# Optimization experiments

Measured on AMD Instinct MI355X. Metric: run time of the kernel, lower is better.

The kernel has to match this reference:

```python
import jax, jax.numpy as jnp
import numpy as np

B, S, D = 32, 4096, 512

def setup_inputs() -> dict:
    key = jax.random.key(0)
    ks = jax.random.split(key, 5)
    scale = 1.0 / np.sqrt(D)
    return {
        "query": jax.random.normal(ks[0], (B, D), jnp.float32),
        "values": jax.random.normal(ks[1], (B, S, D), jnp.float32),
        "W1": jax.random.normal(ks[2], (D, D), jnp.float32) * scale,
        "b1": jnp.zeros((D,), jnp.float32),
        "W2": jax.random.normal(ks[3], (D, D), jnp.float32) * scale,
        "b2": jnp.zeros((D,), jnp.float32),
        "V": jax.random.normal(ks[4], (D, 1), jnp.float32) * scale,
        "bv": jnp.zeros((1,), jnp.float32),
    }

def reference(query, values, W1, b1, W2, b2, V, bv):
    # query: [B, D], values: [B, S, D]
    q_proj = query @ W1 + b1                      # [B, D]
    v_proj = jnp.einsum('bsd,de->bse', values, W2) + b2  # [B, S, D]
    hidden = jnp.tanh(q_proj[:, None, :] + v_proj)       # [B, S, D]
    score = jnp.einsum('bsd,de->bse', hidden, V) + bv    # [B, S, 1]
    attn = jax.nn.softmax(score, axis=1)                 # softmax over seq axis
    context = jnp.sum(attn * values, axis=1)             # [B, D]
    return (context, attn)
```

## Files before the change

kernel.cpp:

```cpp
#include <hip/hip_runtime.h>
#include <hip/hip_bf16.h>
#include <stdint.h>

#define NB 32
#define NS 4096
#define ND 512

typedef __attribute__((ext_vector_type(8))) short short8;
typedef __attribute__((ext_vector_type(4))) float floatx4;

__device__ __forceinline__ short f2bf(float f) {
    unsigned int u = __builtin_bit_cast(unsigned int, f);
    return (short)((u + 0x8000u) >> 16);
}

__device__ __forceinline__ float fast_tanh(float x) {
    float e = __expf(2.0f * x);
    return 1.0f - 2.0f * __builtin_amdgcn_rcpf(e + 1.0f);
}

__device__ __forceinline__ short8 pack8(float4 a, float4 b) {
    short8 w;
    w[0] = f2bf(a.x); w[1] = f2bf(a.y); w[2] = f2bf(a.z); w[3] = f2bf(a.w);
    w[4] = f2bf(b.x); w[5] = f2bf(b.y); w[6] = f2bf(b.z); w[7] = f2bf(b.w);
    return w;
}

__global__ void __launch_bounds__(256) qproj_kernel(
    const float* __restrict__ query, const float* __restrict__ W1,
    const float* __restrict__ b1, const float* __restrict__ b2,
    float* __restrict__ qb) {
    int b = blockIdx.x;
    int t = threadIdx.x;
    __shared__ float q[ND];
    q[t] = query[b * ND + t];
    q[t + 256] = query[b * ND + t + 256];
    __syncthreads();
    float acc0 = 0.f, acc1 = 0.f;
#pragma unroll 8
    for (int k = 0; k < ND; k++) {
        float qk = q[k];
        acc0 += qk * W1[k * ND + t];
        acc1 += qk * W1[k * ND + t + 256];
    }
    qb[b * ND + t] = acc0 + b1[t] + b2[t];
    qb[b * ND + t + 256] = acc1 + b1[t + 256] + b2[t + 256];
}

__global__ void __launch_bounds__(256) w2t_kernel(
    const float* __restrict__ W2, unsigned short* __restrict__ W2Tt) {
    int g = blockIdx.x * 256 + threadIdx.x;
    int nt = g >> 14;
    int ks = (g >> 10) & 15;
    int kq = (g >> 8) & 3;
    int n  = g & 255;
    int e  = nt * 256 + n;
    int k0 = ks * 32 + kq * 8;
    short8 v;
#pragma unroll
    for (int j = 0; j < 8; j++)
        v[j] = f2bf(W2[(size_t)(k0 + j) * ND + e]);
    *(short8*)&W2Tt[(size_t)g * 8] = v;
}

__global__ void __launch_bounds__(256, 2) scores_kernel(
    const float* __restrict__ values, const unsigned short* __restrict__ W2Tt,
    const float* __restrict__ qb, const float* __restrict__ V,
    float* __restrict__ scores) {
    const int nt = blockIdx.x;
    const int st = blockIdx.y;
    const int b  = blockIdx.z;
    const int n0 = nt * 256, s0 = st * 128;

    __shared__ __align__(16) unsigned short sA[2][4096];
    __shared__ __align__(16) unsigned short sB[2][8192];
    __shared__ float sQb[256];
    __shared__ float sV[256];

    const int tid  = threadIdx.x;
    const int lane = tid & 63;
    const int wave = tid >> 6;
    const int wr = wave >> 1, wc = wave & 1;
    const int mr = lane & 15;
    const int q  = lane >> 4;

    sQb[tid] = qb[b * ND + n0 + tid];
    sV[tid]  = V[n0 + tid];

    floatx4 acc[4][8] = {};

    const int arow = tid >> 1, ah = tid & 1;
    const float* arow_ptr = values + ((size_t)b * NS + s0 + arow) * ND + ah * 16;
    const int awr0 = (2 * ah * 128 + arow) * 8;
    const int awr1 = ((2 * ah + 1) * 128 + arow) * 8;

    const unsigned short* bsrc0 = W2Tt + (size_t)(nt * 16) * 8192;

    const int aoff = (q * 128 + wr * 64 + mr) * 8;
    const int boff = (q * 256 + wc * 128 + mr) * 8;

    {
#pragma unroll
        for (int r = 0; r < 4; r++) {
            int c = tid + 256 * r;
            __builtin_amdgcn_global_load_lds(
                (const __attribute__((address_space(1))) unsigned int*)(bsrc0 + c * 8),
                (__attribute__((address_space(3))) unsigned int*)&sB[0][c * 8],
                16, 0, 0);
        }
        const float4* ap = (const float4*)arow_ptr;
        float4 x0 = ap[0], x1 = ap[1], x2 = ap[2], x3 = ap[3];
        *(short8*)&sA[0][awr0] = pack8(x0, x1);
        *(short8*)&sA[0][awr1] = pack8(x2, x3);
    }
    __syncthreads();

    for (int ks = 0; ks < 16; ks++) {
        const int cur = ks & 1, nxt = cur ^ 1;
        float4 x0, x1, x2, x3;
        if (ks < 15) {
            const unsigned short* bsrc = bsrc0 + (size_t)(ks + 1) * 8192;
#pragma unroll
            for (int r = 0; r < 4; r++) {
                int c = tid + 256 * r;
                __builtin_amdgcn_global_load_lds(
                    (const __attribute__((address_space(1))) unsigned int*)(bsrc + c * 8),
                    (__attribute__((address_space(3))) unsigned int*)&sB[nxt][c * 8],
                    16, 0, 0);
            }
            const float4* ap = (const float4*)(arow_ptr + (ks + 1) * 32);
            x0 = ap[0]; x1 = ap[1]; x2 = ap[2]; x3 = ap[3];
        }

        short8 af[4], bfr[8];
#pragma unroll
        for (int i = 0; i < 4; i++) af[i]  = *(const short8*)&sA[cur][aoff + i * 128];
#pragma unroll
        for (int j = 0; j < 8; j++) bfr[j] = *(const short8*)&sB[cur][boff + j * 128];
#pragma unroll
        for (int i = 0; i < 4; i++)
#pragma unroll
            for (int j = 0; j < 8; j++)
                acc[i][j] = __builtin_amdgcn_mfma_f32_16x16x32_bf16(af[i], bfr[j], acc[i][j], 0, 0, 0);

        if (ks < 15) {
            *(short8*)&sA[nxt][awr0] = pack8(x0, x1);
            *(short8*)&sA[nxt][awr1] = pack8(x2, x3);
        }
        __syncthreads();
    }

    float vcoef[8], qadd[8];
#pragma unroll
    for (int j = 0; j < 8; j++) {
        int col = wc * 128 + j * 16 + mr;
        vcoef[j] = sV[col];
        qadd[j]  = sQb[col];
    }

#pragma unroll
    for (int i = 0; i < 4; i++) {
#pragma unroll
        for (int r = 0; r < 4; r++) {
            float p = 0.f;
#pragma unroll
            for (int j = 0; j < 8; j++)
                p += fast_tanh(acc[i][j][r] + qadd[j]) * vcoef[j];
            p += __shfl_xor(p, 1);
            p += __shfl_xor(p, 2);
            p += __shfl_xor(p, 4);
            p += __shfl_xor(p, 8);
            if (mr == 0) {
                int row = wr * 64 + i * 16 + q * 4 + r;
                atomicAdd(&scores[(size_t)b * NS + s0 + row], p);
            }
        }
    }
}

__global__ void __launch_bounds__(256) softmax_kernel(
    const float* __restrict__ scores, float* __restrict__ attn) {
    int b = blockIdx.x;
    int t = threadIdx.x;
    __shared__ float red[4];
    __shared__ float bcast[2];
    const float* sc = scores + (size_t)b * NS;
    float v[16];
    float m = -1e30f;
#pragma unroll
    for (int i = 0; i < 16; i++) { v[i] = sc[t + i * 256]; m = fmaxf(m, v[i]); }
    for (int o = 32; o; o >>= 1) m = fmaxf(m, __shfl_xor(m, o));
    if ((t & 63) == 0) red[t >> 6] = m;
    __syncthreads();
    if (t == 0) bcast[0] = fmaxf(fmaxf(red[0], red[1]), fmaxf(red[2], red[3]));
    __syncthreads();
    m = bcast[0];
    float sum = 0.f;
#pragma unroll
    for (int i = 0; i < 16; i++) { v[i] = __expf(v[i] - m); sum += v[i]; }
    for (int o = 32; o; o >>= 1) sum += __shfl_xor(sum, o);
    if ((t & 63) == 0) red[t >> 6] = sum;
    __syncthreads();
    if (t == 0) bcast[1] = red[0] + red[1] + red[2] + red[3];
    __syncthreads();
    float inv = 1.0f / bcast[1];
    float* ao = attn + (size_t)b * NS;
#pragma unroll
    for (int i = 0; i < 16; i++) ao[t + i * 256] = v[i] * inv;
}

__global__ void __launch_bounds__(256) context_partial_kernel(
    const float* __restrict__ values, const float* __restrict__ attn,
    float* __restrict__ pctx) {
    int sc = blockIdx.x;
    int b  = blockIdx.y;
    int t  = threadIdx.x;
    __shared__ float sAttn[512];
    sAttn[t]       = attn[(size_t)b * NS + sc * 512 + t];
    sAttn[t + 256] = attn[(size_t)b * NS + sc * 512 + t + 256];
    __syncthreads();
    int d = t * 2;
    const float2* vp = (const float2*)(values + ((size_t)b * NS + sc * 512) * ND + d);
    float ax = 0.f, ay = 0.f;
#pragma unroll 8
    for (int s = 0; s < 512; s++) {
        float a = sAttn[s];
        float2 v = vp[(size_t)s * 256];
        ax += a * v.x; ay += a * v.y;
    }
    pctx[((size_t)sc * 32 + b) * ND + d]     = ax;
    pctx[((size_t)sc * 32 + b) * ND + d + 1] = ay;
}

__global__ void __launch_bounds__(256) context_reduce_kernel(
    const float* __restrict__ pctx, float* __restrict__ ctx) {
    int i = blockIdx.x * 256 + threadIdx.x;
    float s = 0.f;
#pragma unroll
    for (int p = 0; p < 8; p++) s += pctx[(size_t)p * (32 * ND) + i];
    ctx[i] = s;
}

extern "C" void kernel_launch(void* const* d_in, const int* in_sizes, int n_in,
                              void* d_out, int out_size, void* d_ws, size_t ws_size,
                              hipStream_t stream) {
    const float* query  = (const float*)d_in[0];
    const float* values = (const float*)d_in[1];
    const float* W1     = (const float*)d_in[2];
    const float* b1     = (const float*)d_in[3];
    const float* W2     = (const float*)d_in[4];
    const float* b2     = (const float*)d_in[5];
    const float* V      = (const float*)d_in[6];

    float* ctx_out  = (float*)d_out;
    float* attn_out = (float*)d_out + NB * ND;

    char* ws = (char*)d_ws;
    float*          qb     = (float*)ws;
    unsigned short* W2Tt   = (unsigned short*)(ws + (64 << 10));
    float*          scores = (float*)(ws + (64 << 10) + (512 << 10));
    float*          pctx   = (float*)(ws + (64 << 10) + (1024 << 10));

    hipMemsetAsync(scores, 0, (size_t)NB * NS * sizeof(float), stream);

    qproj_kernel<<<NB, 256, 0, stream>>>(query, W1, b1, b2, qb);
    w2t_kernel<<<128, 256, 0, stream>>>(W2, W2Tt);
    scores_kernel<<<dim3(2, 32, 32), 256, 0, stream>>>(values, W2Tt, qb, V, scores);
    softmax_kernel<<<NB, 256, 0, stream>>>(scores, attn_out);
    context_partial_kernel<<<dim3(8, 32), 256, 0, stream>>>(values, attn_out, pctx);
    context_reduce_kernel<<<64, 256, 0, stream>>>(pctx, ctx_out);
}
```

Measured before the change: 535.0 us.

## Stream fp32 values tiles directly into LDS and shrink score tile to 64 rows

The scores kernel now copies fp32 values tiles straight into LDS with global_load_lds, using an XOR-swizzled layout, and converts them to bf16 when building MFMA fragments. It no longer loads into registers, packs, and stores to LDS. The sequence tile is halved to 64 rows, each wave covers 64 output columns, and occupancy is raised to 3 blocks. The aim is to overlap the A-tile load asynchronously and get more blocks in flight. In exchange, each block reuses the B tile over fewer rows, and bf16 conversion is repeated at fragment time. The qproj kernel is also split over an extra grid dimension with a k-split reduction to use more blocks.

```diff
diff --git a/kernel.cpp b/kernel.cpp
--- a/kernel.cpp
+++ b/kernel.cpp
@@ -17,34 +17,34 @@
 __device__ __forceinline__ float fast_tanh(float x) {
     float e = __expf(2.0f * x);
     return 1.0f - 2.0f * __builtin_amdgcn_rcpf(e + 1.0f);
-}
-
-__device__ __forceinline__ short8 pack8(float4 a, float4 b) {
-    short8 w;
-    w[0] = f2bf(a.x); w[1] = f2bf(a.y); w[2] = f2bf(a.z); w[3] = f2bf(a.w);
-    w[4] = f2bf(b.x); w[5] = f2bf(b.y); w[6] = f2bf(b.z); w[7] = f2bf(b.w);
-    return w;
 }
 
 __global__ void __launch_bounds__(256) qproj_kernel(
     const float* __restrict__ query, const float* __restrict__ W1,
     const float* __restrict__ b1, const float* __restrict__ b2,
     float* __restrict__ qb) {
-    int b = blockIdx.x;
-    int t = threadIdx.x;
+    const int b  = blockIdx.x;
+    const int es = blockIdx.y;
+    const int t  = threadIdx.x;
+    const int col = t & 63, kc = t >> 6;
     __shared__ float q[ND];
+    __shared__ float red[256];
     q[t] = query[b * ND + t];
     q[t + 256] = query[b * ND + t + 256];
     __syncthreads();
-    float acc0 = 0.f, acc1 = 0.f;
+    float acc = 0.f;
+    const float* wp = W1 + (size_t)(kc * 128) * ND + es * 64 + col;
+    const float* qp = q + kc * 128;
 #pragma unroll 8
-    for (int k = 0; k < ND; k++) {
-        float qk = q[k];
-        acc0 += qk * W1[k * ND + t];
-        acc1 += qk * W1[k * ND + t + 256];
-    }
-    qb[b * ND + t] = acc0 + b1[t] + b2[t];
-    qb[b * ND + t + 256] = acc1 + b1[t + 256] + b2[t + 256];
+    for (int k = 0; k < 128; k++)
+        acc += qp[k] * wp[(size_t)k * ND];
+    red[t] = acc;
+    __syncthreads();
+    if (t < 64) {
+        float s = red[t] + red[t + 64] + red[t + 128] + red[t + 192];
+        int e = es * 64 + t;
+        qb[b * ND + e] = s + b1[e] + b2[e];
+    }
 }
 
 __global__ void __launch_bounds__(256) w2t_kernel(
@@ -63,16 +63,16 @@
     *(short8*)&W2Tt[(size_t)g * 8] = v;
 }
 
-__global__ void __launch_bounds__(256, 2) scores_kernel(
+__global__ void __launch_bounds__(256, 3) scores_kernel(
     const float* __restrict__ values, const unsigned short* __restrict__ W2Tt,
     const float* __restrict__ qb, const float* __restrict__ V,
     float* __restrict__ scores) {
     const int nt = blockIdx.x;
     const int st = blockIdx.y;
     const int b  = blockIdx.z;
-    const int n0 = nt * 256, s0 = st * 128;
-
-    __shared__ __align__(16) unsigned short sA[2][4096];
+    const int n0 = nt * 256, s0 = st * 64;
+
+    __shared__ __align__(16) float sA[2][2048];
     __shared__ __align__(16) unsigned short sB[2][8192];
     __shared__ float sQb[256];
     __shared__ float sV[256];
@@ -80,46 +80,59 @@
     const int tid  = threadIdx.x;
     const int lane = tid & 63;
     const int wave = tid >> 6;
-    const int wr = wave >> 1, wc = wave & 1;
     const int mr = lane & 15;
     const int q  = lane >> 4;
 
     sQb[tid] = qb[b * ND + n0 + tid];
     sV[tid]  = V[n0 + tid];
 
-    floatx4 acc[4][8] = {};
-
-    const int arow = tid >> 1, ah = tid & 1;
-    const float* arow_ptr = values + ((size_t)b * NS + s0 + arow) * ND + ah * 16;
-    const int awr0 = (2 * ah * 128 + arow) * 8;
-    const int awr1 = ((2 * ah + 1) * 128 + arow) * 8;
-
-    const unsigned short* bsrc0 = W2Tt + (size_t)(nt * 16) * 8192;
-
-    const int aoff = (q * 128 + wr * 64 + mr) * 8;
-    const int boff = (q * 256 + wc * 128 + mr) * 8;
-
-    {
-#pragma unroll
-        for (int r = 0; r < 4; r++) {
-            int c = tid + 256 * r;
-            __builtin_amdgcn_global_load_lds(
-                (const __attribute__((address_space(1))) unsigned int*)(bsrc0 + c * 8),
-                (__attribute__((address_space(3))) unsigned int*)&sB[0][c * 8],
-                16, 0, 0);
-        }
-        const float4* ap = (const float4*)arow_ptr;
-        float4 x0 = ap[0], x1 = ap[1], x2 = ap[2], x3 = ap[3];
-        *(short8*)&sA[0][awr0] = pack8(x0, x1);
-        *(short8*)&sA[0][awr1] = pack8(x2, x3);
+    floatx4 acc[4][4] = {};
+
+    const float* abase = values + ((size_t)b * NS + s0) * ND;
+    const unsigned short* bbase = W2Tt + (size_t)(nt * 16) * 8192;
+
+#pragma unroll
+    for (int r = 0; r < 4; r++) {
+        int c = tid + 256 * r;
+        __builtin_amdgcn_global_load_lds(
+            (const __attribute__((address_space(1))) unsigned int*)(bbase + c * 8),
+            (__attribute__((address_space(3))) unsigned int*)&sB[0][c * 8],
+            16, 0, 0);
+    }
+#pragma unroll
+    for (int r = 0; r < 2; r++) {
+        int c = tid + 256 * r;
+        int row = c >> 3;
+        int kq4 = (c & 7) ^ (row & 7);
+        __builtin_amdgcn_global_load_lds(
+            (const __attribute__((address_space(1))) unsigned int*)(abase + (size_t)row * ND + kq4 * 4),
+            (__attribute__((address_space(3))) unsigned int*)&sA[0][c * 4],
+            16, 0, 0);
     }
     __syncthreads();
 
     for (int ks = 0; ks < 16; ks++) {
         const int cur = ks & 1, nxt = cur ^ 1;
-        float4 x0, x1, x2, x3;
+
+        short8 af[4], bfr[4];
+#pragma unroll
+        for (int i = 0; i < 4; i++) {
+            int row = i * 16 + mr;
+            int c0 = row * 8 + ((2 * q) ^ (mr & 7));
+            float4 f0 = *(const float4*)&sA[cur][c0 * 4];
+            float4 f1 = *(const float4*)&sA[cur][(c0 ^ 1) * 4];
+            short8 a;
+            a[0] = f2bf(f0.x); a[1] = f2bf(f0.y); a[2] = f2bf(f0.z); a[3] = f2bf(f0.w);
+            a[4] = f2bf(f1.x); a[5] = f2bf(f1.y); a[6] = f2bf(f1.z); a[7] = f2bf(f1.w);
+            af[i] = a;
+        }
+#pragma unroll
+        for (int j = 0; j < 4; j++)
+            bfr[j] = *(const short8*)&sB[cur][(q * 256 + wave * 64 + j * 16 + mr) * 8];
+
         if (ks < 15) {
-            const unsigned short* bsrc = bsrc0 + (size_t)(ks + 1) * 8192;
+            const unsigned short* bsrc = bbase + (size_t)(ks + 1) * 8192;
+            const float* asrc = abase + (ks + 1) * 32;
 #pragma unroll
             for (int r = 0; r < 4; r++) {
                 int c = tid + 256 * r;
@@ -128,32 +141,31 @@
                     (__attribute__((address_space(3))) unsigned int*)&sB[nxt][c * 8],
                     16, 0, 0);
             }
-            const float4* ap = (const float4*)(arow_ptr + (ks + 1) * 32);
-            x0 = ap[0]; x1 = ap[1]; x2 = ap[2]; x3 = ap[3];
+#pragma unroll
+            for (int r = 0; r < 2; r++) {
+                int c = tid + 256 * r;
+                int row = c >> 3;
+                int kq4 = (c & 7) ^ (row & 7);
+                __builtin_amdgcn_global_load_lds(
+                    (const __attribute__((address_space(1))) unsigned int*)(asrc + (size_t)row * ND + kq4 * 4),
+                    (__attribute__((address_space(3))) unsigned int*)&sA[nxt][c * 4],
+                    16, 0, 0);
+            }
         }
 
-        short8 af[4], bfr[8];
-#pragma unroll
-        for (int i = 0; i < 4; i++) af[i]  = *(const short8*)&sA[cur][aoff + i * 128];
-#pragma unroll
-        for (int j = 0; j < 8; j++) bfr[j] = *(const short8*)&sB[cur][boff + j * 128];
 #pragma unroll
         for (int i = 0; i < 4; i++)
 #pragma unroll
-            for (int j = 0; j < 8; j++)
+            for (int j = 0; j < 4; j++)
                 acc[i][j] = __builtin_amdgcn_mfma_f32_16x16x32_bf16(af[i], bfr[j], acc[i][j], 0, 0, 0);
 
-        if (ks < 15) {
-            *(short8*)&sA[nxt][awr0] = pack8(x0, x1);
-            *(short8*)&sA[nxt][awr1] = pack8(x2, x3);
-        }
         __syncthreads();
     }
 
-    float vcoef[8], qadd[8];
-#pragma unroll
-    for (int j = 0; j < 8; j++) {
-        int col = wc * 128 + j * 16 + mr;
+    float vcoef[4], qadd[4];
+#pragma unroll
+    for (int j = 0; j < 4; j++) {
+        int col = wave * 64 + j * 16 + mr;
         vcoef[j] = sV[col];
         qadd[j]  = sQb[col];
     }
@@ -164,14 +176,14 @@
         for (int r = 0; r < 4; r++) {
             float p = 0.f;
 #pragma unroll
-            for (int j = 0; j < 8; j++)
+            for (int j = 0; j < 4; j++)
                 p += fast_tanh(acc[i][j][r] + qadd[j]) * vcoef[j];
             p += __shfl_xor(p, 1);
             p += __shfl_xor(p, 2);
             p += __shfl_xor(p, 4);
             p += __shfl_xor(p, 8);
             if (mr == 0) {
-                int row = wr * 64 + i * 16 + q * 4 + r;
+                int row = i * 16 + q * 4 + r;
                 atomicAdd(&scores[(size_t)b * NS + s0 + row], p);
             }
         }
@@ -263,9 +275,9 @@
 
     hipMemsetAsync(scores, 0, (size_t)NB * NS * sizeof(float), stream);
 
-    qproj_kernel<<<NB, 256, 0, stream>>>(query, W1, b1, b2, qb);
+    qproj_kernel<<<dim3(NB, 8), 256, 0, stream>>>(query, W1, b1, b2, qb);
     w2t_kernel<<<128, 256, 0, stream>>>(W2, W2Tt);
-    scores_kernel<<<dim3(2, 32, 32), 256, 0, stream>>>(values, W2Tt, qb, V, scores);
+    scores_kernel<<<dim3(2, 64, 32), 256, 0, stream>>>(values, W2Tt, qb, V, scores);
     softmax_kernel<<<NB, 256, 0, stream>>>(scores, attn_out);
     context_partial_kernel<<<dim3(8, 32), 256, 0, stream>>>(values, attn_out, pctx);
     context_reduce_kernel<<<64, 256, 0, stream>>>(pctx, ctx_out);
```

Measured after the change: 498.3 us. -6.9%, faster.

## Pre-convert values to tiled bf16 and triple-buffer async loads in scores kernel

Applied to the files above, without the earlier changes.

Adds a pass that converts values once to bf16 in a k-slab-major tiled layout. The scores kernel can then stream both operands into LDS with global_load_lds through a three-stage ring guarded by explicit waitcnt and barriers, instead of loading fp32 in registers and packing it inline. The context kernel now reads the bf16 copy, split across k-slabs with an in-block reduction, and qproj is split over output column groups for more parallelism. The cost is an extra full read/write pass over values, lower precision in the context sum, and a larger workspace.

```diff
diff --git a/kernel.cpp b/kernel.cpp
--- a/kernel.cpp
+++ b/kernel.cpp
@@ -30,21 +30,28 @@
     const float* __restrict__ query, const float* __restrict__ W1,
     const float* __restrict__ b1, const float* __restrict__ b2,
     float* __restrict__ qb) {
-    int b = blockIdx.x;
-    int t = threadIdx.x;
+    const int b  = blockIdx.x;
+    const int es = blockIdx.y;
+    const int t  = threadIdx.x;
+    const int col = t & 63, kc = t >> 6;
     __shared__ float q[ND];
+    __shared__ float red[256];
     q[t] = query[b * ND + t];
     q[t + 256] = query[b * ND + t + 256];
     __syncthreads();
-    float acc0 = 0.f, acc1 = 0.f;
+    float acc = 0.f;
+    const float* wp = W1 + (size_t)(kc * 128) * ND + es * 64 + col;
+    const float* qp = q + kc * 128;
 #pragma unroll 8
-    for (int k = 0; k < ND; k++) {
-        float qk = q[k];
-        acc0 += qk * W1[k * ND + t];
-        acc1 += qk * W1[k * ND + t + 256];
-    }
-    qb[b * ND + t] = acc0 + b1[t] + b2[t];
-    qb[b * ND + t + 256] = acc1 + b1[t + 256] + b2[t + 256];
+    for (int k = 0; k < 128; k++)
+        acc += qp[k] * wp[(size_t)k * ND];
+    red[t] = acc;
+    __syncthreads();
+    if (t < 64) {
+        float s = red[t] + red[t + 64] + red[t + 128] + red[t + 192];
+        int e = es * 64 + t;
+        qb[b * ND + e] = s + b1[e] + b2[e];
+    }
 }
 
 __global__ void __launch_bounds__(256) w2t_kernel(
@@ -63,8 +70,40 @@
     *(short8*)&W2Tt[(size_t)g * 8] = v;
 }
 
+__global__ void __launch_bounds__(256) vconv_kernel(
+    const float* __restrict__ values, unsigned short* __restrict__ vbfT) {
+    size_t g = (size_t)blockIdx.x * 256 + threadIdx.x;
+    int kk = (int)(g & 63);
+    size_t bs = g >> 6;
+    int b = (int)(bs >> 12), s = (int)(bs & 4095);
+    const float4* src = (const float4*)(values + g * 8);
+    float4 x0 = src[0], x1 = src[1];
+    short8 w = pack8(x0, x1);
+    int ks = kk >> 2, kq = kk & 3;
+    *(short8*)&vbfT[((size_t)(b * 16 + ks) * 4096 + s) * 32 + kq * 8] = w;
+}
+
+__device__ __forceinline__ void stage_step(
+    const unsigned short* bsrc, const unsigned short* asrc,
+    unsigned short* sB, unsigned short* sA, int tid) {
+#pragma unroll
+    for (int r = 0; r < 4; r++) {
+        int c = tid + 256 * r;
+        __builtin_amdgcn_global_load_lds(
+            (const __attribute__((address_space(1))) unsigned int*)(bsrc + c * 8),
+            (__attribute__((address_space(3))) unsigned int*)(sB + c * 8), 16, 0, 0);
+    }
+#pragma unroll
+    for (int r = 0; r < 2; r++) {
+        int c = tid + 256 * r;
+        __builtin_amdgcn_global_load_lds(
+            (const __attribute__((address_space(1))) unsigned int*)(asrc + c * 8),
+            (__attribute__((address_space(3))) unsigned int*)(sA + c * 8), 16, 0, 0);
+    }
+}
+
 __global__ void __launch_bounds__(256, 2) scores_kernel(
-    const float* __restrict__ values, const unsigned short* __restrict__ W2Tt,
+    const unsigned short* __restrict__ vbfT, const unsigned short* __restrict__ W2Tt,
     const float* __restrict__ qb, const float* __restrict__ V,
     float* __restrict__ scores) {
     const int nt = blockIdx.x;
@@ -72,8 +111,8 @@
     const int b  = blockIdx.z;
     const int n0 = nt * 256, s0 = st * 128;
 
-    __shared__ __align__(16) unsigned short sA[2][4096];
-    __shared__ __align__(16) unsigned short sB[2][8192];
+    __shared__ __align__(16) unsigned short sA[3][4096];
+    __shared__ __align__(16) unsigned short sB[3][8192];
     __shared__ float sQb[256];
     __shared__ float sV[256];
 
@@ -86,68 +125,46 @@
 
     sQb[tid] = qb[b * ND + n0 + tid];
     sV[tid]  = V[n0 + tid];
+    __syncthreads();
+
+    const unsigned short* aplane = vbfT + (size_t)b * 16 * 131072 + (size_t)s0 * 32;
+    const unsigned short* bbase  = W2Tt + (size_t)nt * 131072;
 
     floatx4 acc[4][8] = {};
 
-    const int arow = tid >> 1, ah = tid & 1;
-    const float* arow_ptr = values + ((size_t)b * NS + s0 + arow) * ND + ah * 16;
-    const int awr0 = (2 * ah * 128 + arow) * 8;
-    const int awr1 = ((2 * ah + 1) * 128 + arow) * 8;
-
-    const unsigned short* bsrc0 = W2Tt + (size_t)(nt * 16) * 8192;
-
-    const int aoff = (q * 128 + wr * 64 + mr) * 8;
+    stage_step(bbase, aplane, &sB[0][0], &sA[0][0], tid);
+    stage_step(bbase + 8192, aplane + 131072, &sB[1][0], &sA[1][0], tid);
+
+    const int aoff = (wr * 64 + mr) * 32 + q * 8;
     const int boff = (q * 256 + wc * 128 + mr) * 8;
 
-    {
-#pragma unroll
-        for (int r = 0; r < 4; r++) {
-            int c = tid + 256 * r;
-            __builtin_amdgcn_global_load_lds(
-                (const __attribute__((address_space(1))) unsigned int*)(bsrc0 + c * 8),
-                (__attribute__((address_space(3))) unsigned int*)&sB[0][c * 8],
-                16, 0, 0);
+#pragma unroll
+    for (int ks = 0; ks < 16; ks++) {
+        if (ks == 15) __builtin_amdgcn_s_waitcnt(0x0F70);
+        else          __builtin_amdgcn_s_waitcnt(0x0F76);
+        __builtin_amdgcn_s_barrier();
+        __builtin_amdgcn_sched_barrier(0);
+
+        const int cur = ks % 3;
+        short8 af[4], bfr[8];
+#pragma unroll
+        for (int i = 0; i < 4; i++)
+            af[i] = *(const short8*)&sA[cur][aoff + i * 512];
+#pragma unroll
+        for (int j = 0; j < 8; j++)
+            bfr[j] = *(const short8*)&sB[cur][boff + j * 128];
+
+        if (ks < 14) {
+            stage_step(bbase + (size_t)(ks + 2) * 8192,
+                       aplane + (size_t)(ks + 2) * 131072,
+                       &sB[(ks + 2) % 3][0], &sA[(ks + 2) % 3][0], tid);
         }
-        const float4* ap = (const float4*)arow_ptr;
-        float4 x0 = ap[0], x1 = ap[1], x2 = ap[2], x3 = ap[3];
-        *(short8*)&sA[0][awr0] = pack8(x0, x1);
-        *(short8*)&sA[0][awr1] = pack8(x2, x3);
-    }
-    __syncthreads();
-
-    for (int ks = 0; ks < 16; ks++) {
-        const int cur = ks & 1, nxt = cur ^ 1;
-        float4 x0, x1, x2, x3;
-        if (ks < 15) {
-            const unsigned short* bsrc = bsrc0 + (size_t)(ks + 1) * 8192;
-#pragma unroll
-            for (int r = 0; r < 4; r++) {
-                int c = tid + 256 * r;
-                __builtin_amdgcn_global_load_lds(
-                    (const __attribute__((address_space(1))) unsigned int*)(bsrc + c * 8),
-                    (__attribute__((address_space(3))) unsigned int*)&sB[nxt][c * 8],
-                    16, 0, 0);
-            }
-            const float4* ap = (const float4*)(arow_ptr + (ks + 1) * 32);
-            x0 = ap[0]; x1 = ap[1]; x2 = ap[2]; x3 = ap[3];
-        }
-
-        short8 af[4], bfr[8];
-#pragma unroll
-        for (int i = 0; i < 4; i++) af[i]  = *(const short8*)&sA[cur][aoff + i * 128];
-#pragma unroll
-        for (int j = 0; j < 8; j++) bfr[j] = *(const short8*)&sB[cur][boff + j * 128];
+
 #pragma unroll
         for (int i = 0; i < 4; i++)
 #pragma unroll
             for (int j = 0; j < 8; j++)
                 acc[i][j] = __builtin_amdgcn_mfma_f32_16x16x32_bf16(af[i], bfr[j], acc[i][j], 0, 0, 0);
-
-        if (ks < 15) {
-            *(short8*)&sA[nxt][awr0] = pack8(x0, x1);
-            *(short8*)&sA[nxt][awr1] = pack8(x2, x3);
-        }
-        __syncthreads();
     }
 
     float vcoef[8], qadd[8];
@@ -157,7 +174,6 @@
         vcoef[j] = sV[col];
         qadd[j]  = sQb[col];
     }
-
 #pragma unroll
     for (int i = 0; i < 4; i++) {
 #pragma unroll
@@ -210,26 +226,39 @@
 }
 
 __global__ void __launch_bounds__(256) context_partial_kernel(
-    const float* __restrict__ values, const float* __restrict__ attn,
+    const unsigned short* __restrict__ vbfT, const float* __restrict__ attn,
     float* __restrict__ pctx) {
-    int sc = blockIdx.x;
-    int b  = blockIdx.y;
-    int t  = threadIdx.x;
+    const int ks = blockIdx.x;
+    const int sc = blockIdx.y;
+    const int b  = blockIdx.z;
+    const int t  = threadIdx.x;
     __shared__ float sAttn[512];
+    __shared__ float redx[256], redy[256];
     sAttn[t]       = attn[(size_t)b * NS + sc * 512 + t];
     sAttn[t + 256] = attn[(size_t)b * NS + sc * 512 + t + 256];
     __syncthreads();
-    int d = t * 2;
-    const float2* vp = (const float2*)(values + ((size_t)b * NS + sc * 512) * ND + d);
+    const int dpair = t & 15, spar = t >> 4;
+    const unsigned short* plane = vbfT + ((size_t)(b * 16 + ks) * 4096 + sc * 512) * 32;
     float ax = 0.f, ay = 0.f;
-#pragma unroll 8
-    for (int s = 0; s < 512; s++) {
+#pragma unroll 4
+    for (int i = 0; i < 32; i++) {
+        int s = spar + 16 * i;
+        unsigned int u = *(const unsigned int*)&plane[(size_t)s * 32 + dpair * 2];
+        float vx = __builtin_bit_cast(float, u << 16);
+        float vy = __builtin_bit_cast(float, u & 0xFFFF0000u);
         float a = sAttn[s];
-        float2 v = vp[(size_t)s * 256];
-        ax += a * v.x; ay += a * v.y;
-    }
-    pctx[((size_t)sc * 32 + b) * ND + d]     = ax;
-    pctx[((size_t)sc * 32 + b) * ND + d + 1] = ay;
+        ax += a * vx; ay += a * vy;
+    }
+    redx[t] = ax; redy[t] = ay;
+    __syncthreads();
+    if (t < 16) {
+        float sx = 0.f, sy = 0.f;
+#pragma unroll
+        for (int sp = 0; sp < 16; sp++) { sx += redx[sp * 16 + t]; sy += redy[sp * 16 + t]; }
+        int d = ks * 32 + t * 2;
+        pctx[((size_t)sc * 32 + b) * ND + d]     = sx;
+        pctx[((size_t)sc * 32 + b) * ND + d + 1] = sy;
+    }
 }
 
 __global__ void __launch_bounds__(256) context_reduce_kernel(
@@ -256,17 +285,20 @@
     float* attn_out = (float*)d_out + NB * ND;
 
     char* ws = (char*)d_ws;
-    float*          qb     = (float*)ws;
-    unsigned short* W2Tt   = (unsigned short*)(ws + (64 << 10));
-    float*          scores = (float*)(ws + (64 << 10) + (512 << 10));
-    float*          pctx   = (float*)(ws + (64 << 10) + (1024 << 10));
+    unsigned short* vbfT   = (unsigned short*)ws;
+    const size_t VB = (size_t)NB * NS * ND * 2;
+    float*          qb     = (float*)(ws + VB);
+    unsigned short* W2Tt   = (unsigned short*)(ws + VB + (64 << 10));
+    float*          scores = (float*)(ws + VB + (576 << 10));
+    float*          pctx   = (float*)(ws + VB + (1088 << 10));
 
     hipMemsetAsync(scores, 0, (size_t)NB * NS * sizeof(float), stream);
 
-    qproj_kernel<<<NB, 256, 0, stream>>>(query, W1, b1, b2, qb);
+    vconv_kernel<<<32768, 256, 0, stream>>>(values, vbfT);
     w2t_kernel<<<128, 256, 0, stream>>>(W2, W2Tt);
-    scores_kernel<<<dim3(2, 32, 32), 256, 0, stream>>>(values, W2Tt, qb, V, scores);
+    qproj_kernel<<<dim3(NB, 8), 256, 0, stream>>>(query, W1, b1, b2, qb);
+    scores_kernel<<<dim3(2, 32, 32), 256, 0, stream>>>(vbfT, W2Tt, qb, V, scores);
     softmax_kernel<<<NB, 256, 0, stream>>>(scores, attn_out);
-    context_partial_kernel<<<dim3(8, 32), 256, 0, stream>>>(values, attn_out, pctx);
+    context_partial_kernel<<<dim3(16, 8, 32), 256, 0, stream>>>(vbfT, attn_out, pctx);
     context_reduce_kernel<<<64, 256, 0, stream>>>(pctx, ctx_out);
 }
```

Measured after the change: 500.6 us. 1.07x faster.
